# Kernel tuning notes

Hardware: AMD Instinct MI355X
Metric: run time of the kernel (lower is better)

Reference implementation:

```python
import jax, jax.numpy as jnp
import numpy as np

D, H = 64, 16
B, S = 4, 4096
PI = 3.1415  # constant used verbatim in the original code


def setup_inputs() -> dict:
    key = jax.random.key(0)
    ks = jax.random.split(key, 11)
    inp = {
        'query': jax.random.normal(ks[0], (B, S, D), dtype=jnp.float32),
        'key': jax.random.normal(ks[1], (B, S, D), dtype=jnp.float32),
        'value': jax.random.normal(ks[2], (B, S, D), dtype=jnp.float32),
        'attn_mask': jnp.zeros((1,), dtype=bool),
        # Linear weights stored as (in, out); y = x @ W + b
        'wq_w': jax.random.normal(ks[3], (D, D * H), dtype=jnp.float32) * 0.05,
        'wq_b': jnp.zeros((D * H,), dtype=jnp.float32),
        'wk_w': jax.random.normal(ks[4], (D, D * H), dtype=jnp.float32) * 0.05,
        'wk_b': jnp.zeros((D * H,), dtype=jnp.float32),
        'wv_w': jax.random.normal(ks[5], (D, D * H), dtype=jnp.float32) * 0.05,
        'wv_b': jnp.zeros((D * H,), dtype=jnp.float32),
        'dense_w': jax.random.normal(ks[6], (D * H, D), dtype=jnp.float32) * 0.05,
        'dense_b': jnp.zeros((D,), dtype=jnp.float32),
    }
    return inp


def reference(query, key, value, attn_mask, wq_w, wq_b, wk_w, wk_b, wv_w, wv_b, dense_w, dense_b):
    b, s, _ = query.shape
    # projections -> (B, S, H, D); einsum axis n = heads
    q = (query @ wq_w + wq_b).reshape(b, s, H, D)
    k = (key @ wk_w + wk_b).reshape(b, s, H, D)
    v = (value @ wv_w + wv_b).reshape(b, s, H, D)

    q = jax.nn.elu(q) + 1.0
    k = jax.nn.elu(k) + 1.0

    pos = PI * jnp.arange(s, dtype=query.dtype) / s  # (S,)
    qc_w = jnp.cos(pos)
    qs_w = jnp.sin(pos)
    kc_w = jnp.sin(pos)  # NB: original uses sin for k_cos too (faithful)
    ks_w = jnp.sin(pos)

    q_cos = q * qc_w[None, :, None, None]
    q_sin = q * qs_w[None, :, None, None]
    k_cos = k * kc_w[None, :, None, None]
    k_sin = k * ks_w[None, :, None, None]

    def lin_attn(qf, kf):
        kv = jnp.einsum('bsnx,bsnz->bnxz', kf, v)      # (B,H,D,D)
        return jnp.einsum('bsnx,bnxz->bsnz', qf, kv)   # (B,S,H,D)

    qkv = lin_attn(q, k)
    qkv_cos = lin_attn(q_cos, k_cos)
    qkv_sin = lin_attn(q_sin, k_sin)

    denom = 1.0 / (
        jnp.einsum('bsnd,bnd->bsn', q, k.sum(axis=1))
        + jnp.einsum('bsnd,bnd->bsn', q_cos, k_cos.sum(axis=1))
        + jnp.einsum('bsnd,bnd->bsn', q_sin, k_sin.sum(axis=1))
        + 1e-05
    )

    O = (qkv + qkv_cos + qkv_sin) * denom[..., None]   # (B,S,H,D)
    concat = O.reshape(b, s, H * D)
    return concat @ dense_w + dense_b
```

## Files before the change

kernel.cpp:

```cpp
#include <hip/hip_runtime.h>
#include <math.h>

#define BB 4
#define SS 4096
#define DD 64
#define HH 16
#define PI_C 3.1415f


typedef __attribute__((ext_vector_type(8))) short short8;
typedef __attribute__((ext_vector_type(4))) float f32x4;

#define MFMA(a, b, c) __builtin_amdgcn_mfma_f32_16x16x32_bf16(a, b, c, 0, 0, 0)

__device__ __forceinline__ short f2bf(float f) {
    union { float f; unsigned u; } v; v.f = f;
    unsigned r = v.u + 0x7FFFu + ((v.u >> 16) & 1u);
    return (short)(r >> 16);
}
__device__ __forceinline__ float bf2f(short s) {
    union { unsigned u; float f; } v;
    v.u = ((unsigned)(unsigned short)s) << 16;
    return v.f;
}
__device__ __forceinline__ short8 cvt8(float4 a, float4 b) {
    short8 r;
    r[0] = f2bf(a.x); r[1] = f2bf(a.y); r[2] = f2bf(a.z); r[3] = f2bf(a.w);
    r[4] = f2bf(b.x); r[5] = f2bf(b.y); r[6] = f2bf(b.z); r[7] = f2bf(b.w);
    return r;
}
__device__ __forceinline__ float elu1(float x) { return x > 0.f ? x + 1.f : __expf(x); }
__device__ __forceinline__ void st4(short* p, short a, short b, short c, short d) {
    union { uint2 u; short s[4]; } x;
    x.s[0] = a; x.s[1] = b; x.s[2] = c; x.s[3] = d;
    *reinterpret_cast<uint2*>(p) = x.u;
}

__global__ __launch_bounds__(256) void k_prep(
    const float* __restrict__ wq, const float* __restrict__ wk,
    const float* __restrict__ wv, const float* __restrict__ wd,
    short* __restrict__ dst)
{
    const int h = blockIdx.x, y = blockIdx.y, t = threadIdx.x;
    const float* src = (y == 0) ? wq : (y == 1) ? wk : (y == 2) ? wv : wd;
    const int rs = (y < 3) ? 1024 : 64;
    const size_t srcbase = (y < 3) ? (size_t)(h * 64) : (size_t)(h * 4096);
    short* dm = dst + (size_t)y * 65536 + (size_t)h * 4096;
#pragma unroll
    for (int j = 0; j < 4; ++j) {
        int idx = j * 1024 + t * 4;
        int r = idx >> 6, c = idx & 63;
        float4 v = *reinterpret_cast<const float4*>(src + (size_t)r * rs + srcbase + c);
        dm[(c + 0) * 64 + r] = f2bf(v.x);
        dm[(c + 1) * 64 + r] = f2bf(v.y);
        dm[(c + 2) * 64 + r] = f2bf(v.z);
        dm[(c + 3) * 64 + r] = f2bf(v.w);
    }
}

__global__ __launch_bounds__(256, 2) void k_phase1(
    const float* __restrict__ key, const float* __restrict__ value,
    const float* __restrict__ wk_b, const float* __restrict__ wv_b,
    const short* __restrict__ wkTb, const short* __restrict__ wvTb,
    float* __restrict__ pkv, float* __restrict__ pkvs,
    float* __restrict__ pks)
{
    const int chunk = blockIdx.x, h = blockIdx.y, b = blockIdx.z;
    const int t = threadIdx.x, w = t >> 6, l = t & 63;
    const int lane15 = l & 15, q8 = (l >> 4) * 8, q4 = (l >> 4) * 4;

    __shared__ short kT[64 * 72], vT[64 * 72], vsT[64 * 72];
    __shared__ float ssin[512];
    __shared__ float sbk[64], sbv[64];
    __shared__ float sred[512];

    short8 bkf[2][4], bvf[2][4];
    {
        const short* wkh = wkTb + (size_t)h * 4096;
        const short* wvh = wvTb + (size_t)h * 4096;
#pragma unroll
        for (int kss = 0; kss < 2; ++kss)
#pragma unroll
            for (int nt = 0; nt < 4; ++nt) {
                bkf[kss][nt] = *reinterpret_cast<const short8*>(wkh + (nt * 16 + lane15) * 64 + kss * 32 + q8);
                bvf[kss][nt] = *reinterpret_cast<const short8*>(wvh + (nt * 16 + lane15) * 64 + kss * 32 + q8);
            }
    }
    ssin[t]       = __sinf(PI_C * (float)(chunk * 512 + t)       * (1.f / 4096.f));
    ssin[t + 256] = __sinf(PI_C * (float)(chunk * 512 + t + 256) * (1.f / 4096.f));
    if (t < 64) sbk[t] = wk_b[h * 64 + t];
    else if (t < 128) sbv[t - 64] = wv_b[h * 64 + (t - 64)];

    float4 kf0, kf1, kf2, kf3, vf0, vf1, vf2, vf3;
    {
        const size_t g = ((size_t)b * SS + chunk * 512 + w * 16 + lane15) * 64 + q8;
        kf0 = *reinterpret_cast<const float4*>(key + g);
        kf1 = *reinterpret_cast<const float4*>(key + g + 4);
        kf2 = *reinterpret_cast<const float4*>(key + g + 32);
        kf3 = *reinterpret_cast<const float4*>(key + g + 36);
        vf0 = *reinterpret_cast<const float4*>(value + g);
        vf1 = *reinterpret_cast<const float4*>(value + g + 4);
        vf2 = *reinterpret_cast<const float4*>(value + g + 32);
        vf3 = *reinterpret_cast<const float4*>(value + g + 36);
    }

    f32x4 ckv[4], ckvs[4];
#pragma unroll
    for (int i = 0; i < 4; ++i) {
        ckv[i]  = (f32x4){0.f, 0.f, 0.f, 0.f};
        ckvs[i] = (f32x4){0.f, 0.f, 0.f, 0.f};
    }
    float aks = 0.f, akss = 0.f;
    __syncthreads();

    for (int it = 0; it < 8; ++it) {
        const int sbase = it * 64;
        f32x4 ckp[4], cvp[4];
#pragma unroll
        for (int i = 0; i < 4; ++i) {
            ckp[i] = (f32x4){0.f, 0.f, 0.f, 0.f};
            cvp[i] = (f32x4){0.f, 0.f, 0.f, 0.f};
        }
        {
            short8 ak0 = cvt8(kf0, kf1), ak1 = cvt8(kf2, kf3);
            short8 av0 = cvt8(vf0, vf1), av1 = cvt8(vf2, vf3);
#pragma unroll
            for (int nt = 0; nt < 4; ++nt) {
                ckp[nt] = MFMA(ak0, bkf[0][nt], ckp[nt]);
                cvp[nt] = MFMA(av0, bvf[0][nt], cvp[nt]);
                ckp[nt] = MFMA(ak1, bkf[1][nt], ckp[nt]);
                cvp[nt] = MFMA(av1, bvf[1][nt], cvp[nt]);
            }
        }
        const int srel = w * 16 + q4;
#pragma unroll
        for (int nt = 0; nt < 4; ++nt) {
            const int x = nt * 16 + lane15;
            const float bk = sbk[x], bv = sbv[x];
            short ek[4], ev[4], es[4];
#pragma unroll
            for (int r = 0; r < 4; ++r) {
                float kk = elu1(ckp[nt][r] + bk);
                float vv = cvp[nt][r] + bv;
                ek[r] = f2bf(kk);
                ev[r] = f2bf(vv);
                es[r] = f2bf(vv * ssin[sbase + srel + r]);
            }
            st4(&kT [x * 72 + srel], ek[0], ek[1], ek[2], ek[3]);
            st4(&vT [x * 72 + srel], ev[0], ev[1], ev[2], ev[3]);
            st4(&vsT[x * 72 + srel], es[0], es[1], es[2], es[3]);
        }
        __syncthreads();
        if (it < 7) {
            const size_t g = ((size_t)b * SS + chunk * 512 + (it + 1) * 64 + w * 16 + lane15) * 64 + q8;
            kf0 = *reinterpret_cast<const float4*>(key + g);
            kf1 = *reinterpret_cast<const float4*>(key + g + 4);
            kf2 = *reinterpret_cast<const float4*>(key + g + 32);
            kf3 = *reinterpret_cast<const float4*>(key + g + 36);
            vf0 = *reinterpret_cast<const float4*>(value + g);
            vf1 = *reinterpret_cast<const float4*>(value + g + 4);
            vf2 = *reinterpret_cast<const float4*>(value + g + 32);
            vf3 = *reinterpret_cast<const float4*>(value + g + 36);
        }
#pragma unroll
        for (int kstep = 0; kstep < 2; ++kstep) {
            const int so = kstep * 32;
            short8 aV  = *reinterpret_cast<const short8*>(&vT [(w * 16 + lane15) * 72 + so + q8]);
            short8 aVS = *reinterpret_cast<const short8*>(&vsT[(w * 16 + lane15) * 72 + so + q8]);
#pragma unroll
            for (int nt = 0; nt < 4; ++nt) {
                short8 bK = *reinterpret_cast<const short8*>(&kT[(nt * 16 + lane15) * 72 + so + q8]);
                ckv[nt]  = MFMA(aV,  bK, ckv[nt]);
                ckvs[nt] = MFMA(aVS, bK, ckvs[nt]);
            }
        }
        {
            short8 k0 = *reinterpret_cast<const short8*>(&kT[l * 72 + w * 16]);
            short8 k1 = *reinterpret_cast<const short8*>(&kT[l * 72 + w * 16 + 8]);
#pragma unroll
            for (int e = 0; e < 8; ++e) {
                float fa = bf2f(k0[e]), fb = bf2f(k1[e]);
                aks  += fa + fb;
                akss += fa * ssin[sbase + w * 16 + e] + fb * ssin[sbase + w * 16 + 8 + e];
            }
        }
        __syncthreads();
    }

    const int bh = b * HH + h;
    const size_t pbase = ((size_t)(chunk * 64) + bh) * 4096;
#pragma unroll
    for (int nt = 0; nt < 4; ++nt) {
        const int x = nt * 16 + lane15;
#pragma unroll
        for (int r = 0; r < 4; ++r) {
            const int z = w * 16 + q4 + r;
            pkv [pbase + z * 64 + x] = ckv[nt][r];
            pkvs[pbase + z * 64 + x] = ckvs[nt][r];
        }
    }
    sred[t] = aks; sred[256 + t] = akss;
    __syncthreads();
    if (t < 64) {
        pks[((size_t)(chunk * 64) + bh) * 128 + t] =
            sred[t] + sred[64 + t] + sred[128 + t] + sred[192 + t];
    } else if (t < 128) {
        int tt = t - 64;
        pks[((size_t)(chunk * 64) + bh) * 128 + t] =
            sred[256 + tt] + sred[320 + tt] + sred[384 + tt] + sred[448 + tt];
    }
}

__global__ __launch_bounds__(256) void k_reduce(
    const float* __restrict__ pkv, const float* __restrict__ pkvs,
    const float* __restrict__ pks,
    short* __restrict__ kvb, short* __restrict__ kvsb,
    float* __restrict__ ksums)
{
    const int blk = blockIdx.x, t = threadIdx.x;
    if (blk < 512) {
        const float* src = (blk < 256) ? pkv : pkvs;
        short* dst = (blk < 256) ? kvb : kvsb;
        const int o4 = (blk & 255) * 256 + t;
        float4 s = make_float4(0.f, 0.f, 0.f, 0.f);
#pragma unroll
        for (int c = 0; c < 8; ++c) {
            float4 v = reinterpret_cast<const float4*>(src + (size_t)c * 262144)[o4];
            s.x += v.x; s.y += v.y; s.z += v.z; s.w += v.w;
        }
        st4(dst + (size_t)o4 * 4, f2bf(s.x), f2bf(s.y), f2bf(s.z), f2bf(s.w));
    } else {
        const int g = (blk - 512) * 256 + t;
        float4 s = make_float4(0.f, 0.f, 0.f, 0.f);
#pragma unroll
        for (int c = 0; c < 8; ++c) {
            float4 v = reinterpret_cast<const float4*>(pks + (size_t)c * 8192)[g];
            s.x += v.x; s.y += v.y; s.z += v.z; s.w += v.w;
        }
        reinterpret_cast<float4*>(ksums)[g] = s;
    }
}

__global__ __launch_bounds__(256, 4) void k_phase2(
    const float* __restrict__ query, const float* __restrict__ wq_b,
    const short* __restrict__ wqTb,
    const short* __restrict__ kvb, const short* __restrict__ kvsb,
    const float* __restrict__ ksums,
    const short* __restrict__ wdTb, const float* __restrict__ dense_b,
    float* __restrict__ out)
{
    const int st = blockIdx.x, b = blockIdx.y;
    const int s0 = st * 16;
    const int t = threadIdx.x, w = t >> 6, l = t & 63;
    const int lane15 = l & 15, q8 = (l >> 4) * 8, q4 = (l >> 4) * 4;
    const int x = w * 16 + lane15;

    __shared__ short sqin[16 * 72], sqp[16 * 72], sO[16 * 72];
    __shared__ float sbq[1024];
    __shared__ float sks2[128];
    __shared__ float scc[16], sdb[64];

    if (t < 128) {
        int row = t >> 3, c8 = (t & 7) * 8;
        const float* qp = query + ((size_t)b * SS + s0 + row) * 64 + c8;
        float4 f0 = *reinterpret_cast<const float4*>(qp);
        float4 f1 = *reinterpret_cast<const float4*>(qp + 4);
        *reinterpret_cast<short8*>(&sqin[row * 72 + c8]) = cvt8(f0, f1);
    }
    for (int i = t; i < 1024; i += 256) sbq[i] = wq_b[i];
    if (t < 16) {
        float p = PI_C * (float)(s0 + t) * (1.f / 4096.f);
        scc[t] = __cosf(p) + __sinf(p);
    }
    if (t >= 192) sdb[t - 192] = dense_b[t - 192];
    f32x4 cd = (f32x4){0.f, 0.f, 0.f, 0.f};
    __syncthreads();

    for (int h = 0; h < HH; ++h) {
        const size_t bh = (size_t)(b * HH + h);
        if (t < 128) sks2[t] = ksums[bh * 128 + t];

        f32x4 cq = (f32x4){0.f, 0.f, 0.f, 0.f};
        const short* wqh = wqTb + bh % HH * 0 + (size_t)h * 4096;
#pragma unroll
        for (int kss = 0; kss < 2; ++kss) {
            short8 a = *reinterpret_cast<const short8*>(&sqin[lane15 * 72 + kss * 32 + q8]);
            short8 bb = *reinterpret_cast<const short8*>(wqh + x * 64 + kss * 32 + q8);
            cq = MFMA(a, bb, cq);
        }
        short8 nb1[2], nb2[2];
#pragma unroll
        for (int kss = 0; kss < 2; ++kss) {
            nb1[kss] = *reinterpret_cast<const short8*>(kvb  + bh * 4096 + x * 64 + kss * 32 + q8);
            nb2[kss] = *reinterpret_cast<const short8*>(kvsb + bh * 4096 + x * 64 + kss * 32 + q8);
        }
        {
            const float bq = sbq[h * 64 + x];
#pragma unroll
            for (int r = 0; r < 4; ++r)
                sqp[(q4 + r) * 72 + x] = f2bf(elu1(cq[r] + bq));
        }
        __syncthreads();

        float invd;
        {
            const int sl = l >> 2;
            const int x0 = (l & 3) * 16;
            const float ccs = scc[sl];
            short8 qa = *reinterpret_cast<const short8*>(&sqp[sl * 72 + x0]);
            short8 qb = *reinterpret_cast<const short8*>(&sqp[sl * 72 + x0 + 8]);
            float dsum = 0.f;
#pragma unroll
            for (int e = 0; e < 8; ++e) {
                dsum += bf2f(qa[e]) * (sks2[x0 + e]     + ccs * sks2[64 + x0 + e]);
                dsum += bf2f(qb[e]) * (sks2[x0 + 8 + e] + ccs * sks2[64 + x0 + 8 + e]);
            }
            dsum += __shfl_xor(dsum, 1);
            dsum += __shfl_xor(dsum, 2);
            invd = 1.f / (dsum + 1e-5f);
        }
        float invq[4], ccq[4];
#pragma unroll
        for (int r = 0; r < 4; ++r) {
            invq[r] = __shfl(invd, (q4 + r) * 4);
            ccq[r]  = scc[q4 + r];
        }

        f32x4 ckv = (f32x4){0.f, 0.f, 0.f, 0.f};
        f32x4 ckvs = (f32x4){0.f, 0.f, 0.f, 0.f};
#pragma unroll
        for (int kss = 0; kss < 2; ++kss) {
            short8 a = *reinterpret_cast<const short8*>(&sqp[lane15 * 72 + kss * 32 + q8]);
            ckv  = MFMA(a, nb1[kss], ckv);
            ckvs = MFMA(a, nb2[kss], ckvs);
        }
        short8 dbf[2];
#pragma unroll
        for (int kss = 0; kss < 2; ++kss)
            dbf[kss] = *reinterpret_cast<const short8*>(wdTb + (size_t)h * 4096 + x * 64 + kss * 32 + q8);
#pragma unroll
        for (int r = 0; r < 4; ++r) {
            float o = (ckv[r] + ccq[r] * ckvs[r]) * invq[r];
            sO[(q4 + r) * 72 + x] = f2bf(o);
        }
        __syncthreads();

#pragma unroll
        for (int kss = 0; kss < 2; ++kss) {
            short8 a = *reinterpret_cast<const short8*>(&sO[lane15 * 72 + kss * 32 + q8]);
            cd = MFMA(a, dbf[kss], cd);
        }
    }

    {
        const float bias = sdb[x];
#pragma unroll
        for (int r = 0; r < 4; ++r)
            out[((size_t)b * SS + s0 + q4 + r) * 64 + x] = cd[r] + bias;
    }
}

extern "C" void kernel_launch(void* const* d_in, const int* in_sizes, int n_in,
                              void* d_out, int out_size, void* d_ws, size_t ws_size,
                              hipStream_t stream) {
    const float* query   = (const float*)d_in[0];
    const float* key     = (const float*)d_in[1];
    const float* value   = (const float*)d_in[2];
    const float* wq_w    = (const float*)d_in[4];
    const float* wq_b    = (const float*)d_in[5];
    const float* wk_w    = (const float*)d_in[6];
    const float* wk_b    = (const float*)d_in[7];
    const float* wv_w    = (const float*)d_in[8];
    const float* wv_b    = (const float*)d_in[9];
    const float* dense_w = (const float*)d_in[10];
    const float* dense_b = (const float*)d_in[11];
    float* out = (float*)d_out;

    char* ws = (char*)d_ws;
    float* pkv   = (float*)(ws);
    float* pkvs  = (float*)(ws + 8388608);
    float* pks   = (float*)(ws + 16777216);
    short* kvb   = (short*)(ws + 17039360);
    short* kvsb  = (short*)(ws + 17563648);
    float* ksums = (float*)(ws + 18087936);
    short* wT    = (short*)(ws + 18120704);
    short* wqTb  = wT;
    short* wkTb  = wT + 65536;
    short* wvTb  = wT + 131072;
    short* wdTb  = wT + 196608;

    hipLaunchKernelGGL(k_prep, dim3(16, 4), dim3(256), 0, stream,
                       wq_w, wk_w, wv_w, dense_w, wT);
    hipLaunchKernelGGL(k_phase1, dim3(8, HH, BB), dim3(256), 0, stream,
                       key, value, wk_b, wv_b, wkTb, wvTb, pkv, pkvs, pks);
    hipLaunchKernelGGL(k_reduce, dim3(520), dim3(256), 0, stream,
                       pkv, pkvs, pks, kvb, kvsb, ksums);
    hipLaunchKernelGGL(k_phase2, dim3(256, BB), dim3(256), 0, stream,
                       query, wq_b, wqTb, kvb, kvsb, ksums, wdTb, dense_b, out);
}
```

Baseline: 173.7 us.

## Split phase1 into K/V warp groups with double-buffered LDS; per-warp heads in phase2

Phase1 now runs 512 threads per block. Four warps project and transform K while four warps handle V, and the LDS tiles are double-buffered so the next tile's projection overlaps the current kv accumulation, which removes one barrier per iteration. Phase2 no longer loops over all 16 heads with block-wide barriers. Each warp processes 4 heads independently in a private LDS buffer, computes the denominator via shuffles from preloaded ksums, and the warps' partial dense outputs are reduced through shared memory at the end. This raises LDS usage and register pressure per block, and phase2's launch bounds are loosened to 3 blocks per CU.

```diff
diff --git a/kernel.cpp b/kernel.cpp
--- a/kernel.cpp
+++ b/kernel.cpp
@@ -58,7 +58,7 @@
     }
 }
 
-__global__ __launch_bounds__(256, 2) void k_phase1(
+__global__ __launch_bounds__(512, 4) void k_phase1(
     const float* __restrict__ key, const float* __restrict__ value,
     const float* __restrict__ wk_b, const float* __restrict__ wv_b,
     const short* __restrict__ wkTb, const short* __restrict__ wvTb,
@@ -68,120 +68,145 @@
     const int chunk = blockIdx.x, h = blockIdx.y, b = blockIdx.z;
     const int t = threadIdx.x, w = t >> 6, l = t & 63;
     const int lane15 = l & 15, q8 = (l >> 4) * 8, q4 = (l >> 4) * 4;
-
-    __shared__ short kT[64 * 72], vT[64 * 72], vsT[64 * 72];
+    const int pw = w & 3;
+    const bool isV = (w >= 4);
+
+    __shared__ short kT[2][64 * 72];
+    __shared__ short vT[2][64 * 72];
+    __shared__ short vsT[2][64 * 72];
     __shared__ float ssin[512];
-    __shared__ float sbk[64], sbv[64];
-    __shared__ float sred[512];
-
-    short8 bkf[2][4], bvf[2][4];
+    __shared__ float sb[128];
+    __shared__ float sred[1024];
+
+    const short* wsrc = (isV ? wvTb : wkTb) + (size_t)h * 4096;
+    short8 bw[2][4];
+#pragma unroll
+    for (int kss = 0; kss < 2; ++kss)
+#pragma unroll
+        for (int nt = 0; nt < 4; ++nt)
+            bw[kss][nt] = *reinterpret_cast<const short8*>(
+                wsrc + (nt * 16 + lane15) * 64 + kss * 32 + q8);
+
+    ssin[t] = __sinf(PI_C * (float)(chunk * 512 + t) * (1.f / 4096.f));
+    if (t < 64) sb[t] = wk_b[h * 64 + t];
+    else if (t < 128) sb[t] = wv_b[h * 64 + (t - 64)];
+    __syncthreads();
+
+    float biasv[4];
+#pragma unroll
+    for (int nt = 0; nt < 4; ++nt)
+        biasv[nt] = sb[(isV ? 64 : 0) + nt * 16 + lane15];
+
+    const float* gsrc = isV ? value : key;
+    const int scol = pw * 16 + q4;
+
+    float4 f0, f1, f2, f3;
     {
-        const short* wkh = wkTb + (size_t)h * 4096;
-        const short* wvh = wvTb + (size_t)h * 4096;
-#pragma unroll
-        for (int kss = 0; kss < 2; ++kss)
+        const size_t g = ((size_t)b * SS + chunk * 512 + pw * 16 + lane15) * 64 + q8;
+        f0 = *reinterpret_cast<const float4*>(gsrc + g);
+        f1 = *reinterpret_cast<const float4*>(gsrc + g + 4);
+        f2 = *reinterpret_cast<const float4*>(gsrc + g + 32);
+        f3 = *reinterpret_cast<const float4*>(gsrc + g + 36);
+    }
+    {
+        short8 a0 = cvt8(f0, f1), a1 = cvt8(f2, f3);
+        f32x4 cp[4];
+#pragma unroll
+        for (int nt = 0; nt < 4; ++nt) cp[nt] = (f32x4){0.f, 0.f, 0.f, 0.f};
+#pragma unroll
+        for (int nt = 0; nt < 4; ++nt) {
+            cp[nt] = MFMA(a0, bw[0][nt], cp[nt]);
+            cp[nt] = MFMA(a1, bw[1][nt], cp[nt]);
+        }
+#pragma unroll
+        for (int nt = 0; nt < 4; ++nt) {
+            const int x = nt * 16 + lane15;
+            if (!isV) {
+                short e[4];
+#pragma unroll
+                for (int r = 0; r < 4; ++r) e[r] = f2bf(elu1(cp[nt][r] + biasv[nt]));
+                st4(&kT[0][x * 72 + scol], e[0], e[1], e[2], e[3]);
+            } else {
+                short ev[4], es[4];
+#pragma unroll
+                for (int r = 0; r < 4; ++r) {
+                    float vv = cp[nt][r] + biasv[nt];
+                    ev[r] = f2bf(vv);
+                    es[r] = f2bf(vv * ssin[scol + r]);
+                }
+                st4(&vT[0][x * 72 + scol], ev[0], ev[1], ev[2], ev[3]);
+                st4(&vsT[0][x * 72 + scol], es[0], es[1], es[2], es[3]);
+            }
+        }
+    }
+    __syncthreads();
+
+    f32x4 cacc[4];
+#pragma unroll
+    for (int nt = 0; nt < 4; ++nt) cacc[nt] = (f32x4){0.f, 0.f, 0.f, 0.f};
+    float aks = 0.f, akss = 0.f;
+
+    for (int it = 0; it < 8; ++it) {
+        const int p = it & 1;
+        if (it < 7) {
+            const size_t g = ((size_t)b * SS + chunk * 512 + (it + 1) * 64 + pw * 16 + lane15) * 64 + q8;
+            f0 = *reinterpret_cast<const float4*>(gsrc + g);
+            f1 = *reinterpret_cast<const float4*>(gsrc + g + 4);
+            f2 = *reinterpret_cast<const float4*>(gsrc + g + 32);
+            f3 = *reinterpret_cast<const float4*>(gsrc + g + 36);
+        }
+        {
+            const short* At = isV ? vsT[p] : vT[p];
+            short8 a0 = *reinterpret_cast<const short8*>(&At[(pw * 16 + lane15) * 72 + q8]);
+            short8 a1 = *reinterpret_cast<const short8*>(&At[(pw * 16 + lane15) * 72 + 32 + q8]);
 #pragma unroll
             for (int nt = 0; nt < 4; ++nt) {
-                bkf[kss][nt] = *reinterpret_cast<const short8*>(wkh + (nt * 16 + lane15) * 64 + kss * 32 + q8);
-                bvf[kss][nt] = *reinterpret_cast<const short8*>(wvh + (nt * 16 + lane15) * 64 + kss * 32 + q8);
-            }
-    }
-    ssin[t]       = __sinf(PI_C * (float)(chunk * 512 + t)       * (1.f / 4096.f));
-    ssin[t + 256] = __sinf(PI_C * (float)(chunk * 512 + t + 256) * (1.f / 4096.f));
-    if (t < 64) sbk[t] = wk_b[h * 64 + t];
-    else if (t < 128) sbv[t - 64] = wv_b[h * 64 + (t - 64)];
-
-    float4 kf0, kf1, kf2, kf3, vf0, vf1, vf2, vf3;
-    {
-        const size_t g = ((size_t)b * SS + chunk * 512 + w * 16 + lane15) * 64 + q8;
-        kf0 = *reinterpret_cast<const float4*>(key + g);
-        kf1 = *reinterpret_cast<const float4*>(key + g + 4);
-        kf2 = *reinterpret_cast<const float4*>(key + g + 32);
-        kf3 = *reinterpret_cast<const float4*>(key + g + 36);
-        vf0 = *reinterpret_cast<const float4*>(value + g);
-        vf1 = *reinterpret_cast<const float4*>(value + g + 4);
-        vf2 = *reinterpret_cast<const float4*>(value + g + 32);
-        vf3 = *reinterpret_cast<const float4*>(value + g + 36);
-    }
-
-    f32x4 ckv[4], ckvs[4];
-#pragma unroll
-    for (int i = 0; i < 4; ++i) {
-        ckv[i]  = (f32x4){0.f, 0.f, 0.f, 0.f};
-        ckvs[i] = (f32x4){0.f, 0.f, 0.f, 0.f};
-    }
-    float aks = 0.f, akss = 0.f;
-    __syncthreads();
-
-    for (int it = 0; it < 8; ++it) {
-        const int sbase = it * 64;
-        f32x4 ckp[4], cvp[4];
-#pragma unroll
-        for (int i = 0; i < 4; ++i) {
-            ckp[i] = (f32x4){0.f, 0.f, 0.f, 0.f};
-            cvp[i] = (f32x4){0.f, 0.f, 0.f, 0.f};
+                short8 b0 = *reinterpret_cast<const short8*>(&kT[p][(nt * 16 + lane15) * 72 + q8]);
+                short8 b1 = *reinterpret_cast<const short8*>(&kT[p][(nt * 16 + lane15) * 72 + 32 + q8]);
+                cacc[nt] = MFMA(a0, b0, cacc[nt]);
+                cacc[nt] = MFMA(a1, b1, cacc[nt]);
+            }
         }
         {
-            short8 ak0 = cvt8(kf0, kf1), ak1 = cvt8(kf2, kf3);
-            short8 av0 = cvt8(vf0, vf1), av1 = cvt8(vf2, vf3);
+            short8 kk = *reinterpret_cast<const short8*>(&kT[p][l * 72 + w * 8]);
+#pragma unroll
+            for (int e = 0; e < 8; ++e) {
+                float f = bf2f(kk[e]);
+                aks += f;
+                akss = fmaf(f, ssin[it * 64 + w * 8 + e], akss);
+            }
+        }
+        if (it < 7) {
+            short8 a0 = cvt8(f0, f1), a1 = cvt8(f2, f3);
+            f32x4 cp[4];
+#pragma unroll
+            for (int nt = 0; nt < 4; ++nt) cp[nt] = (f32x4){0.f, 0.f, 0.f, 0.f};
 #pragma unroll
             for (int nt = 0; nt < 4; ++nt) {
-                ckp[nt] = MFMA(ak0, bkf[0][nt], ckp[nt]);
-                cvp[nt] = MFMA(av0, bvf[0][nt], cvp[nt]);
-                ckp[nt] = MFMA(ak1, bkf[1][nt], ckp[nt]);
-                cvp[nt] = MFMA(av1, bvf[1][nt], cvp[nt]);
-            }
-        }
-        const int srel = w * 16 + q4;
-#pragma unroll
-        for (int nt = 0; nt < 4; ++nt) {
-            const int x = nt * 16 + lane15;
-            const float bk = sbk[x], bv = sbv[x];
-            short ek[4], ev[4], es[4];
-#pragma unroll
-            for (int r = 0; r < 4; ++r) {
-                float kk = elu1(ckp[nt][r] + bk);
-                float vv = cvp[nt][r] + bv;
-                ek[r] = f2bf(kk);
-                ev[r] = f2bf(vv);
-                es[r] = f2bf(vv * ssin[sbase + srel + r]);
-            }
-            st4(&kT [x * 72 + srel], ek[0], ek[1], ek[2], ek[3]);
-            st4(&vT [x * 72 + srel], ev[0], ev[1], ev[2], ev[3]);
-            st4(&vsT[x * 72 + srel], es[0], es[1], es[2], es[3]);
-        }
-        __syncthreads();
-        if (it < 7) {
-            const size_t g = ((size_t)b * SS + chunk * 512 + (it + 1) * 64 + w * 16 + lane15) * 64 + q8;
-            kf0 = *reinterpret_cast<const float4*>(key + g);
-            kf1 = *reinterpret_cast<const float4*>(key + g + 4);
-            kf2 = *reinterpret_cast<const float4*>(key + g + 32);
-            kf3 = *reinterpret_cast<const float4*>(key + g + 36);
-            vf0 = *reinterpret_cast<const float4*>(value + g);
-            vf1 = *reinterpret_cast<const float4*>(value + g + 4);
-            vf2 = *reinterpret_cast<const float4*>(value + g + 32);
-            vf3 = *reinterpret_cast<const float4*>(value + g + 36);
-        }
-#pragma unroll
-        for (int kstep = 0; kstep < 2; ++kstep) {
-            const int so = kstep * 32;
-            short8 aV  = *reinterpret_cast<const short8*>(&vT [(w * 16 + lane15) * 72 + so + q8]);
-            short8 aVS = *reinterpret_cast<const short8*>(&vsT[(w * 16 + lane15) * 72 + so + q8]);
+                cp[nt] = MFMA(a0, bw[0][nt], cp[nt]);
+                cp[nt] = MFMA(a1, bw[1][nt], cp[nt]);
+            }
+            const int pn = p ^ 1;
+            const int sabs = (it + 1) * 64 + scol;
 #pragma unroll
             for (int nt = 0; nt < 4; ++nt) {
-                short8 bK = *reinterpret_cast<const short8*>(&kT[(nt * 16 + lane15) * 72 + so + q8]);
-                ckv[nt]  = MFMA(aV,  bK, ckv[nt]);
-                ckvs[nt] = MFMA(aVS, bK, ckvs[nt]);
-            }
-        }
-        {
-            short8 k0 = *reinterpret_cast<const short8*>(&kT[l * 72 + w * 16]);
-            short8 k1 = *reinterpret_cast<const short8*>(&kT[l * 72 + w * 16 + 8]);
-#pragma unroll
-            for (int e = 0; e < 8; ++e) {
-                float fa = bf2f(k0[e]), fb = bf2f(k1[e]);
-                aks  += fa + fb;
-                akss += fa * ssin[sbase + w * 16 + e] + fb * ssin[sbase + w * 16 + 8 + e];
+                const int x = nt * 16 + lane15;
+                if (!isV) {
+                    short e[4];
+#pragma unroll
+                    for (int r = 0; r < 4; ++r) e[r] = f2bf(elu1(cp[nt][r] + biasv[nt]));
+                    st4(&kT[pn][x * 72 + scol], e[0], e[1], e[2], e[3]);
+                } else {
+                    short ev[4], es[4];
+#pragma unroll
+                    for (int r = 0; r < 4; ++r) {
+                        float vv = cp[nt][r] + biasv[nt];
+                        ev[r] = f2bf(vv);
+                        es[r] = f2bf(vv * ssin[sabs + r]);
+                    }
+                    st4(&vT[pn][x * 72 + scol], ev[0], ev[1], ev[2], ev[3]);
+                    st4(&vsT[pn][x * 72 + scol], es[0], es[1], es[2], es[3]);
+                }
             }
         }
         __syncthreads();
@@ -189,25 +214,29 @@
 
     const int bh = b * HH + h;
     const size_t pbase = ((size_t)(chunk * 64) + bh) * 4096;
+    float* dst = isV ? pkvs : pkv;
 #pragma unroll
     for (int nt = 0; nt < 4; ++nt) {
         const int x = nt * 16 + lane15;
 #pragma unroll
         for (int r = 0; r < 4; ++r) {
-            const int z = w * 16 + q4 + r;
-            pkv [pbase + z * 64 + x] = ckv[nt][r];
-            pkvs[pbase + z * 64 + x] = ckvs[nt][r];
-        }
-    }
-    sred[t] = aks; sred[256 + t] = akss;
+            const int z = pw * 16 + q4 + r;
+            dst[pbase + z * 64 + x] = cacc[nt][r];
+        }
+    }
+    sred[t] = aks; sred[512 + t] = akss;
     __syncthreads();
     if (t < 64) {
-        pks[((size_t)(chunk * 64) + bh) * 128 + t] =
-            sred[t] + sred[64 + t] + sred[128 + t] + sred[192 + t];
+        float s = 0.f;
+#pragma unroll
+        for (int j = 0; j < 8; ++j) s += sred[j * 64 + t];
+        pks[((size_t)(chunk * 64) + bh) * 128 + t] = s;
     } else if (t < 128) {
-        int tt = t - 64;
-        pks[((size_t)(chunk * 64) + bh) * 128 + t] =
-            sred[256 + tt] + sred[320 + tt] + sred[384 + tt] + sred[448 + tt];
+        const int tt = t - 64;
+        float s = 0.f;
+#pragma unroll
+        for (int j = 0; j < 8; ++j) s += sred[512 + j * 64 + tt];
+        pks[((size_t)(chunk * 64) + bh) * 128 + t] = s;
     }
 }
 
@@ -241,7 +270,7 @@
     }
 }
 
-__global__ __launch_bounds__(256, 4) void k_phase2(
+__global__ __launch_bounds__(256, 3) void k_phase2(
     const float* __restrict__ query, const float* __restrict__ wq_b,
     const short* __restrict__ wqTb,
     const short* __restrict__ kvb, const short* __restrict__ kvsb,
@@ -253,110 +282,144 @@
     const int s0 = st * 16;
     const int t = threadIdx.x, w = t >> 6, l = t & 63;
     const int lane15 = l & 15, q8 = (l >> 4) * 8, q4 = (l >> 4) * 4;
-    const int x = w * 16 + lane15;
-
-    __shared__ short sqin[16 * 72], sqp[16 * 72], sO[16 * 72];
+
+    __shared__ short sqin[16 * 72];
+    __shared__ short wbuf[4][16 * 72];
     __shared__ float sbq[1024];
-    __shared__ float sks2[128];
-    __shared__ float scc[16], sdb[64];
+    __shared__ float sksall[16 * 128];
+    __shared__ float scc[16];
+    __shared__ float sdb[64];
+    __shared__ float sred[4][16 * 68];
 
     if (t < 128) {
         int row = t >> 3, c8 = (t & 7) * 8;
         const float* qp = query + ((size_t)b * SS + s0 + row) * 64 + c8;
-        float4 f0 = *reinterpret_cast<const float4*>(qp);
-        float4 f1 = *reinterpret_cast<const float4*>(qp + 4);
-        *reinterpret_cast<short8*>(&sqin[row * 72 + c8]) = cvt8(f0, f1);
+        float4 g0 = *reinterpret_cast<const float4*>(qp);
+        float4 g1 = *reinterpret_cast<const float4*>(qp + 4);
+        *reinterpret_cast<short8*>(&sqin[row * 72 + c8]) = cvt8(g0, g1);
     }
     for (int i = t; i < 1024; i += 256) sbq[i] = wq_b[i];
+    {
+        const float4* src = reinterpret_cast<const float4*>(ksums + (size_t)b * 2048);
+        reinterpret_cast<float4*>(sksall)[t] = src[t];
+        reinterpret_cast<float4*>(sksall)[t + 256] = src[t + 256];
+    }
     if (t < 16) {
         float p = PI_C * (float)(s0 + t) * (1.f / 4096.f);
         scc[t] = __cosf(p) + __sinf(p);
     }
     if (t >= 192) sdb[t - 192] = dense_b[t - 192];
-    f32x4 cd = (f32x4){0.f, 0.f, 0.f, 0.f};
     __syncthreads();
 
-    for (int h = 0; h < HH; ++h) {
+    float ccr[4];
+#pragma unroll
+    for (int r = 0; r < 4; ++r) ccr[r] = scc[q4 + r];
+
+    short* myb = &wbuf[w][0];
+    f32x4 cd[4];
+#pragma unroll
+    for (int nt = 0; nt < 4; ++nt) cd[nt] = (f32x4){0.f, 0.f, 0.f, 0.f};
+
+    for (int hh = 0; hh < 4; ++hh) {
+        const int h = hh * 4 + w;
         const size_t bh = (size_t)(b * HH + h);
-        if (t < 128) sks2[t] = ksums[bh * 128 + t];
-
-        f32x4 cq = (f32x4){0.f, 0.f, 0.f, 0.f};
-        const short* wqh = wqTb + bh % HH * 0 + (size_t)h * 4096;
-#pragma unroll
-        for (int kss = 0; kss < 2; ++kss) {
-            short8 a = *reinterpret_cast<const short8*>(&sqin[lane15 * 72 + kss * 32 + q8]);
-            short8 bb = *reinterpret_cast<const short8*>(wqh + x * 64 + kss * 32 + q8);
-            cq = MFMA(a, bb, cq);
-        }
-        short8 nb1[2], nb2[2];
-#pragma unroll
-        for (int kss = 0; kss < 2; ++kss) {
-            nb1[kss] = *reinterpret_cast<const short8*>(kvb  + bh * 4096 + x * 64 + kss * 32 + q8);
-            nb2[kss] = *reinterpret_cast<const short8*>(kvsb + bh * 4096 + x * 64 + kss * 32 + q8);
-        }
-        {
+        const short* wqh = wqTb + (size_t)h * 4096;
+
+        short8 aq0 = *reinterpret_cast<const short8*>(&sqin[lane15 * 72 + q8]);
+        short8 aq1 = *reinterpret_cast<const short8*>(&sqin[lane15 * 72 + 32 + q8]);
+        f32x4 cq[4];
+#pragma unroll
+        for (int nt = 0; nt < 4; ++nt) cq[nt] = (f32x4){0.f, 0.f, 0.f, 0.f};
+#pragma unroll
+        for (int nt = 0; nt < 4; ++nt) {
+            short8 b0 = *reinterpret_cast<const short8*>(wqh + (nt * 16 + lane15) * 64 + q8);
+            short8 b1 = *reinterpret_cast<const short8*>(wqh + (nt * 16 + lane15) * 64 + 32 + q8);
+            cq[nt] = MFMA(aq0, b0, cq[nt]);
+            cq[nt] = MFMA(aq1, b1, cq[nt]);
+        }
+        float dp[4] = {0.f, 0.f, 0.f, 0.f};
+#pragma unroll
+        for (int nt = 0; nt < 4; ++nt) {
+            const int x = nt * 16 + lane15;
             const float bq = sbq[h * 64 + x];
-#pragma unroll
-            for (int r = 0; r < 4; ++r)
-                sqp[(q4 + r) * 72 + x] = f2bf(elu1(cq[r] + bq));
-        }
-        __syncthreads();
-
-        float invd;
-        {
-            const int sl = l >> 2;
-            const int x0 = (l & 3) * 16;
-            const float ccs = scc[sl];
-            short8 qa = *reinterpret_cast<const short8*>(&sqp[sl * 72 + x0]);
-            short8 qb = *reinterpret_cast<const short8*>(&sqp[sl * 72 + x0 + 8]);
-            float dsum = 0.f;
-#pragma unroll
-            for (int e = 0; e < 8; ++e) {
-                dsum += bf2f(qa[e]) * (sks2[x0 + e]     + ccs * sks2[64 + x0 + e]);
-                dsum += bf2f(qb[e]) * (sks2[x0 + 8 + e] + ccs * sks2[64 + x0 + 8 + e]);
-            }
-            dsum += __shfl_xor(dsum, 1);
-            dsum += __shfl_xor(dsum, 2);
-            invd = 1.f / (dsum + 1e-5f);
-        }
-        float invq[4], ccq[4];
-#pragma unroll
-        for (int r = 0; r < 4; ++r) {
-            invq[r] = __shfl(invd, (q4 + r) * 4);
-            ccq[r]  = scc[q4 + r];
-        }
-
-        f32x4 ckv = (f32x4){0.f, 0.f, 0.f, 0.f};
-        f32x4 ckvs = (f32x4){0.f, 0.f, 0.f, 0.f};
-#pragma unroll
-        for (int kss = 0; kss < 2; ++kss) {
-            short8 a = *reinterpret_cast<const short8*>(&sqp[lane15 * 72 + kss * 32 + q8]);
-            ckv  = MFMA(a, nb1[kss], ckv);
-            ckvs = MFMA(a, nb2[kss], ckvs);
-        }
-        short8 dbf[2];
-#pragma unroll
-        for (int kss = 0; kss < 2; ++kss)
-            dbf[kss] = *reinterpret_cast<const short8*>(wdTb + (size_t)h * 4096 + x * 64 + kss * 32 + q8);
-#pragma unroll
-        for (int r = 0; r < 4; ++r) {
-            float o = (ckv[r] + ccq[r] * ckvs[r]) * invq[r];
-            sO[(q4 + r) * 72 + x] = f2bf(o);
-        }
-        __syncthreads();
-
-#pragma unroll
-        for (int kss = 0; kss < 2; ++kss) {
-            short8 a = *reinterpret_cast<const short8*>(&sO[lane15 * 72 + kss * 32 + q8]);
-            cd = MFMA(a, dbf[kss], cd);
-        }
-    }
-
+            const float ksx = sksall[h * 128 + x];
+            const float kssx = sksall[h * 128 + 64 + x];
+#pragma unroll
+            for (int r = 0; r < 4; ++r) {
+                float qv = elu1(cq[nt][r] + bq);
+                dp[r] = fmaf(qv, fmaf(ccr[r], kssx, ksx), dp[r]);
+                myb[(q4 + r) * 72 + x] = f2bf(qv);
+            }
+        }
+#pragma unroll
+        for (int m = 1; m <= 8; m <<= 1) {
+#pragma unroll
+            for (int r = 0; r < 4; ++r) dp[r] += __shfl_xor(dp[r], m);
+        }
+        float invd[4];
+#pragma unroll
+        for (int r = 0; r < 4; ++r) invd[r] = 1.f / (dp[r] + 1e-5f);
+
+        const short* kvh  = kvb  + bh * 4096;
+        const short* kvsh = kvsb + bh * 4096;
+        short8 a20 = *reinterpret_cast<const short8*>(&myb[lane15 * 72 + q8]);
+        short8 a21 = *reinterpret_cast<const short8*>(&myb[lane15 * 72 + 32 + q8]);
+        f32x4 ckv[4], ckvs[4];
+#pragma unroll
+        for (int nt = 0; nt < 4; ++nt) {
+            ckv[nt] = (f32x4){0.f, 0.f, 0.f, 0.f};
+            ckvs[nt] = (f32x4){0.f, 0.f, 0.f, 0.f};
+        }
+#pragma unroll
+        for (int nt = 0; nt < 4; ++nt) {
+            short8 b0 = *reinterpret_cast<const short8*>(kvh + (nt * 16 + lane15) * 64 + q8);
+            short8 b1 = *reinterpret_cast<const short8*>(kvh + (nt * 16 + lane15) * 64 + 32 + q8);
+            short8 c0 = *reinterpret_cast<const short8*>(kvsh + (nt * 16 + lane15) * 64 + q8);
+            short8 c1 = *reinterpret_cast<const short8*>(kvsh + (nt * 16 + lane15) * 64 + 32 + q8);
+            ckv[nt]  = MFMA(a20, b0, ckv[nt]);
+            ckv[nt]  = MFMA(a21, b1, ckv[nt]);
+            ckvs[nt] = MFMA(a20, c0, ckvs[nt]);
+            ckvs[nt] = MFMA(a21, c1, ckvs[nt]);
+        }
+#pragma unroll
+        for (int nt = 0; nt < 4; ++nt) {
+            const int z = nt * 16 + lane15;
+#pragma unroll
+            for (int r = 0; r < 4; ++r) {
+                float o = fmaf(ccr[r], ckvs[nt][r], ckv[nt][r]) * invd[r];
+                myb[(q4 + r) * 72 + z] = f2bf(o);
+            }
+        }
+        const short* wdh = wdTb + (size_t)h * 4096;
+        short8 a30 = *reinterpret_cast<const short8*>(&myb[lane15 * 72 + q8]);
+        short8 a31 = *reinterpret_cast<const short8*>(&myb[lane15 * 72 + 32 + q8]);
+#pragma unroll
+        for (int nt = 0; nt < 4; ++nt) {
+            short8 b0 = *reinterpret_cast<const short8*>(wdh + (nt * 16 + lane15) * 64 + q8);
+            short8 b1 = *reinterpret_cast<const short8*>(wdh + (nt * 16 + lane15) * 64 + 32 + q8);
+            cd[nt] = MFMA(a30, b0, cd[nt]);
+            cd[nt] = MFMA(a31, b1, cd[nt]);
+        }
+    }
+
+#pragma unroll
+    for (int nt = 0; nt < 4; ++nt) {
+#pragma unroll
+        for (int r = 0; r < 4; ++r)
+            sred[w][(q4 + r) * 68 + nt * 16 + lane15] = cd[nt][r];
+    }
+    __syncthreads();
     {
-        const float bias = sdb[x];
-#pragma unroll
-        for (int r = 0; r < 4; ++r)
-            out[((size_t)b * SS + s0 + q4 + r) * 64 + x] = cd[r] + bias;
+        const int row = t >> 4, c0 = (t & 15) * 4;
+        float4 s = make_float4(0.f, 0.f, 0.f, 0.f);
+#pragma unroll
+        for (int j = 0; j < 4; ++j) {
+            float4 v = *reinterpret_cast<const float4*>(&sred[j][row * 68 + c0]);
+            s.x += v.x; s.y += v.y; s.z += v.z; s.w += v.w;
+        }
+        float4 db = *reinterpret_cast<const float4*>(&sdb[c0]);
+        s.x += db.x; s.y += db.y; s.z += db.z; s.w += db.w;
+        *reinterpret_cast<float4*>(out + ((size_t)b * SS + s0 + row) * 64 + c0) = s;
     }
 }
 
@@ -391,7 +454,7 @@
 
     hipLaunchKernelGGL(k_prep, dim3(16, 4), dim3(256), 0, stream,
                        wq_w, wk_w, wv_w, dense_w, wT);
-    hipLaunchKernelGGL(k_phase1, dim3(8, HH, BB), dim3(256), 0, stream,
+    hipLaunchKernelGGL(k_phase1, dim3(8, HH, BB), dim3(512), 0, stream,
                        key, value, wk_b, wv_b, wkTb, wvTb, pkv, pkvs, pks);
     hipLaunchKernelGGL(k_reduce, dim3(520), dim3(256), 0, stream,
                        pkv, pkvs, pks, kvb, kvsb, ksums);
```

Result: slower. 206.3 us (+18.8%).

## Split phase-2 across head groups with per-wave heads and partial-sum reduction kernel

Applied to the files above, without the earlier changes.

Replaces the serial 16-head loop in phase 2 with a grid over 4 head groups. Each wave handles one head end to end without block-level syncs, keeping the intermediate tiles in a per-wave LDS buffer. The four wave partials are reduced in LDS and written to a workspace buffer, and a new small kernel sums the group partials and adds the dense bias. This raises parallelism (four times as many blocks) and removes the per-head __syncthreads, at the cost of extra global traffic for the partial sums and one more launch.

```diff
diff --git a/kernel.cpp b/kernel.cpp
--- a/kernel.cpp
+++ b/kernel.cpp
@@ -241,123 +241,167 @@
     }
 }
 
-__global__ __launch_bounds__(256, 4) void k_phase2(
+__global__ __launch_bounds__(256, 2) void k_attn(
     const float* __restrict__ query, const float* __restrict__ wq_b,
     const short* __restrict__ wqTb,
     const short* __restrict__ kvb, const short* __restrict__ kvsb,
     const float* __restrict__ ksums,
-    const short* __restrict__ wdTb, const float* __restrict__ dense_b,
-    float* __restrict__ out)
+    const short* __restrict__ wdTb,
+    float* __restrict__ pden)
 {
-    const int st = blockIdx.x, b = blockIdx.y;
+    const int st = blockIdx.x, g = blockIdx.y, b = blockIdx.z;
     const int s0 = st * 16;
     const int t = threadIdx.x, w = t >> 6, l = t & 63;
     const int lane15 = l & 15, q8 = (l >> 4) * 8, q4 = (l >> 4) * 4;
-    const int x = w * 16 + lane15;
-
-    __shared__ short sqin[16 * 72], sqp[16 * 72], sO[16 * 72];
-    __shared__ float sbq[1024];
-    __shared__ float sks2[128];
-    __shared__ float scc[16], sdb[64];
-
-    if (t < 128) {
-        int row = t >> 3, c8 = (t & 7) * 8;
-        const float* qp = query + ((size_t)b * SS + s0 + row) * 64 + c8;
-        float4 f0 = *reinterpret_cast<const float4*>(qp);
-        float4 f1 = *reinterpret_cast<const float4*>(qp + 4);
-        *reinterpret_cast<short8*>(&sqin[row * 72 + c8]) = cvt8(f0, f1);
-    }
-    for (int i = t; i < 1024; i += 256) sbq[i] = wq_b[i];
-    if (t < 16) {
-        float p = PI_C * (float)(s0 + t) * (1.f / 4096.f);
-        scc[t] = __cosf(p) + __sinf(p);
-    }
-    if (t >= 192) sdb[t - 192] = dense_b[t - 192];
-    f32x4 cd = (f32x4){0.f, 0.f, 0.f, 0.f};
+    const int h = g * 4 + w;
+    const size_t bh = (size_t)(b * HH + h);
+
+    __shared__ short wbuf[4][16 * 72];
+    __shared__ float sred[4][16 * 68];
+
+    short* myb = &wbuf[w][0];
+
+    float ccr[4];
+#pragma unroll
+    for (int r = 0; r < 4; ++r) {
+        float p = PI_C * (float)(s0 + q4 + r) * (1.f / 4096.f);
+        ccr[r] = __cosf(p) + __sinf(p);
+    }
+
+    const float* qrow = query + ((size_t)b * SS + s0 + lane15) * 64;
+    short8 aq0, aq1;
+    {
+        float4 f0 = *reinterpret_cast<const float4*>(qrow + q8);
+        float4 f1 = *reinterpret_cast<const float4*>(qrow + q8 + 4);
+        float4 f2 = *reinterpret_cast<const float4*>(qrow + 32 + q8);
+        float4 f3 = *reinterpret_cast<const float4*>(qrow + 32 + q8 + 4);
+        aq0 = cvt8(f0, f1);
+        aq1 = cvt8(f2, f3);
+    }
+
+    f32x4 cq[4];
+#pragma unroll
+    for (int nt = 0; nt < 4; ++nt) cq[nt] = (f32x4){0.f, 0.f, 0.f, 0.f};
+    {
+        const short* wqh = wqTb + (size_t)h * 4096;
+#pragma unroll
+        for (int nt = 0; nt < 4; ++nt) {
+            short8 b0 = *reinterpret_cast<const short8*>(wqh + (nt * 16 + lane15) * 64 + q8);
+            short8 b1 = *reinterpret_cast<const short8*>(wqh + (nt * 16 + lane15) * 64 + 32 + q8);
+            cq[nt] = MFMA(aq0, b0, cq[nt]);
+            cq[nt] = MFMA(aq1, b1, cq[nt]);
+        }
+    }
+
+    float dp[4] = {0.f, 0.f, 0.f, 0.f};
+#pragma unroll
+    for (int nt = 0; nt < 4; ++nt) {
+        const int x = nt * 16 + lane15;
+        const float bq = wq_b[h * 64 + x];
+        const float ksx = ksums[bh * 128 + x];
+        const float kssx = ksums[bh * 128 + 64 + x];
+#pragma unroll
+        for (int r = 0; r < 4; ++r) {
+            float qv = elu1(cq[nt][r] + bq);
+            dp[r] = fmaf(qv, fmaf(ccr[r], kssx, ksx), dp[r]);
+            myb[(q4 + r) * 72 + x] = f2bf(qv);
+        }
+    }
+#pragma unroll
+    for (int m = 1; m <= 8; m <<= 1) {
+#pragma unroll
+        for (int r = 0; r < 4; ++r) dp[r] += __shfl_xor(dp[r], m);
+    }
+    float invd[4];
+#pragma unroll
+    for (int r = 0; r < 4; ++r) invd[r] = 1.f / (dp[r] + 1e-5f);
+
+    short8 a20 = *reinterpret_cast<const short8*>(&myb[lane15 * 72 + q8]);
+    short8 a21 = *reinterpret_cast<const short8*>(&myb[lane15 * 72 + 32 + q8]);
+
+    f32x4 ckv[4], ckvs[4];
+#pragma unroll
+    for (int nt = 0; nt < 4; ++nt) {
+        ckv[nt]  = (f32x4){0.f, 0.f, 0.f, 0.f};
+        ckvs[nt] = (f32x4){0.f, 0.f, 0.f, 0.f};
+    }
+    {
+        const short* kvh  = kvb  + bh * 4096;
+        const short* kvsh = kvsb + bh * 4096;
+#pragma unroll
+        for (int nt = 0; nt < 4; ++nt) {
+            short8 b0 = *reinterpret_cast<const short8*>(kvh + (nt * 16 + lane15) * 64 + q8);
+            short8 b1 = *reinterpret_cast<const short8*>(kvh + (nt * 16 + lane15) * 64 + 32 + q8);
+            short8 c0 = *reinterpret_cast<const short8*>(kvsh + (nt * 16 + lane15) * 64 + q8);
+            short8 c1 = *reinterpret_cast<const short8*>(kvsh + (nt * 16 + lane15) * 64 + 32 + q8);
+            ckv[nt]  = MFMA(a20, b0, ckv[nt]);
+            ckv[nt]  = MFMA(a21, b1, ckv[nt]);
+            ckvs[nt] = MFMA(a20, c0, ckvs[nt]);
+            ckvs[nt] = MFMA(a21, c1, ckvs[nt]);
+        }
+    }
+
+#pragma unroll
+    for (int nt = 0; nt < 4; ++nt) {
+        const int z = nt * 16 + lane15;
+#pragma unroll
+        for (int r = 0; r < 4; ++r) {
+            float o = fmaf(ccr[r], ckvs[nt][r], ckv[nt][r]) * invd[r];
+            myb[(q4 + r) * 72 + z] = f2bf(o);
+        }
+    }
+    short8 a30 = *reinterpret_cast<const short8*>(&myb[lane15 * 72 + q8]);
+    short8 a31 = *reinterpret_cast<const short8*>(&myb[lane15 * 72 + 32 + q8]);
+
+    f32x4 cd[4];
+#pragma unroll
+    for (int nt = 0; nt < 4; ++nt) cd[nt] = (f32x4){0.f, 0.f, 0.f, 0.f};
+    {
+        const short* wdh = wdTb + (size_t)h * 4096;
+#pragma unroll
+        for (int nt = 0; nt < 4; ++nt) {
+            short8 b0 = *reinterpret_cast<const short8*>(wdh + (nt * 16 + lane15) * 64 + q8);
+            short8 b1 = *reinterpret_cast<const short8*>(wdh + (nt * 16 + lane15) * 64 + 32 + q8);
+            cd[nt] = MFMA(a30, b0, cd[nt]);
+            cd[nt] = MFMA(a31, b1, cd[nt]);
+        }
+    }
+
+#pragma unroll
+    for (int nt = 0; nt < 4; ++nt) {
+#pragma unroll
+        for (int r = 0; r < 4; ++r)
+            sred[w][(q4 + r) * 68 + nt * 16 + lane15] = cd[nt][r];
+    }
     __syncthreads();
-
-    for (int h = 0; h < HH; ++h) {
-        const size_t bh = (size_t)(b * HH + h);
-        if (t < 128) sks2[t] = ksums[bh * 128 + t];
-
-        f32x4 cq = (f32x4){0.f, 0.f, 0.f, 0.f};
-        const short* wqh = wqTb + bh % HH * 0 + (size_t)h * 4096;
-#pragma unroll
-        for (int kss = 0; kss < 2; ++kss) {
-            short8 a = *reinterpret_cast<const short8*>(&sqin[lane15 * 72 + kss * 32 + q8]);
-            short8 bb = *reinterpret_cast<const short8*>(wqh + x * 64 + kss * 32 + q8);
-            cq = MFMA(a, bb, cq);
-        }
-        short8 nb1[2], nb2[2];
-#pragma unroll
-        for (int kss = 0; kss < 2; ++kss) {
-            nb1[kss] = *reinterpret_cast<const short8*>(kvb  + bh * 4096 + x * 64 + kss * 32 + q8);
-            nb2[kss] = *reinterpret_cast<const short8*>(kvsb + bh * 4096 + x * 64 + kss * 32 + q8);
-        }
-        {
-            const float bq = sbq[h * 64 + x];
-#pragma unroll
-            for (int r = 0; r < 4; ++r)
-                sqp[(q4 + r) * 72 + x] = f2bf(elu1(cq[r] + bq));
-        }
-        __syncthreads();
-
-        float invd;
-        {
-            const int sl = l >> 2;
-            const int x0 = (l & 3) * 16;
-            const float ccs = scc[sl];
-            short8 qa = *reinterpret_cast<const short8*>(&sqp[sl * 72 + x0]);
-            short8 qb = *reinterpret_cast<const short8*>(&sqp[sl * 72 + x0 + 8]);
-            float dsum = 0.f;
-#pragma unroll
-            for (int e = 0; e < 8; ++e) {
-                dsum += bf2f(qa[e]) * (sks2[x0 + e]     + ccs * sks2[64 + x0 + e]);
-                dsum += bf2f(qb[e]) * (sks2[x0 + 8 + e] + ccs * sks2[64 + x0 + 8 + e]);
-            }
-            dsum += __shfl_xor(dsum, 1);
-            dsum += __shfl_xor(dsum, 2);
-            invd = 1.f / (dsum + 1e-5f);
-        }
-        float invq[4], ccq[4];
-#pragma unroll
-        for (int r = 0; r < 4; ++r) {
-            invq[r] = __shfl(invd, (q4 + r) * 4);
-            ccq[r]  = scc[q4 + r];
-        }
-
-        f32x4 ckv = (f32x4){0.f, 0.f, 0.f, 0.f};
-        f32x4 ckvs = (f32x4){0.f, 0.f, 0.f, 0.f};
-#pragma unroll
-        for (int kss = 0; kss < 2; ++kss) {
-            short8 a = *reinterpret_cast<const short8*>(&sqp[lane15 * 72 + kss * 32 + q8]);
-            ckv  = MFMA(a, nb1[kss], ckv);
-            ckvs = MFMA(a, nb2[kss], ckvs);
-        }
-        short8 dbf[2];
-#pragma unroll
-        for (int kss = 0; kss < 2; ++kss)
-            dbf[kss] = *reinterpret_cast<const short8*>(wdTb + (size_t)h * 4096 + x * 64 + kss * 32 + q8);
-#pragma unroll
-        for (int r = 0; r < 4; ++r) {
-            float o = (ckv[r] + ccq[r] * ckvs[r]) * invq[r];
-            sO[(q4 + r) * 72 + x] = f2bf(o);
-        }
-        __syncthreads();
-
-#pragma unroll
-        for (int kss = 0; kss < 2; ++kss) {
-            short8 a = *reinterpret_cast<const short8*>(&sO[lane15 * 72 + kss * 32 + q8]);
-            cd = MFMA(a, dbf[kss], cd);
-        }
-    }
-
-    {
-        const float bias = sdb[x];
-#pragma unroll
-        for (int r = 0; r < 4; ++r)
-            out[((size_t)b * SS + s0 + q4 + r) * 64 + x] = cd[r] + bias;
-    }
+    {
+        const int row = t >> 4, c0 = (t & 15) * 4;
+        float4 s = make_float4(0.f, 0.f, 0.f, 0.f);
+#pragma unroll
+        for (int j = 0; j < 4; ++j) {
+            float4 v = *reinterpret_cast<const float4*>(&sred[j][row * 68 + c0]);
+            s.x += v.x; s.y += v.y; s.z += v.z; s.w += v.w;
+        }
+        *reinterpret_cast<float4*>(
+            pden + (((size_t)(g * BB + b) * SS) + s0 + row) * 64 + c0) = s;
+    }
+}
+
+__global__ __launch_bounds__(256) void k_dfinal(
+    const float* __restrict__ pden, const float* __restrict__ dense_b,
+    float* __restrict__ out)
+{
+    const int i4 = blockIdx.x * 256 + threadIdx.x;
+    const int c4 = i4 & 15;
+    const int bb = i4 >> 16;
+    const int rem = i4 & 65535;
+    float4 s = *reinterpret_cast<const float4*>(dense_b + c4 * 4);
+#pragma unroll
+    for (int g = 0; g < 4; ++g) {
+        float4 v = reinterpret_cast<const float4*>(pden)[(size_t)(g * BB + bb) * 65536 + rem];
+        s.x += v.x; s.y += v.y; s.z += v.z; s.w += v.w;
+    }
+    reinterpret_cast<float4*>(out)[i4] = s;
 }
 
 extern "C" void kernel_launch(void* const* d_in, const int* in_sizes, int n_in,
@@ -379,6 +423,7 @@
     char* ws = (char*)d_ws;
     float* pkv   = (float*)(ws);
     float* pkvs  = (float*)(ws + 8388608);
+    float* pden  = (float*)(ws);
     float* pks   = (float*)(ws + 16777216);
     short* kvb   = (short*)(ws + 17039360);
     short* kvsb  = (short*)(ws + 17563648);
@@ -395,6 +440,8 @@
                        key, value, wk_b, wv_b, wkTb, wvTb, pkv, pkvs, pks);
     hipLaunchKernelGGL(k_reduce, dim3(520), dim3(256), 0, stream,
                        pkv, pkvs, pks, kvb, kvsb, ksums);
-    hipLaunchKernelGGL(k_phase2, dim3(256, BB), dim3(256), 0, stream,
-                       query, wq_b, wqTb, kvb, kvsb, ksums, wdTb, dense_b, out);
-}
+    hipLaunchKernelGGL(k_attn, dim3(SS / 16, 4, BB), dim3(256), 0, stream,
+                       query, wq_b, wqTb, kvb, kvsb, ksums, wdTb, pden);
+    hipLaunchKernelGGL(k_dfinal, dim3(1024), dim3(256), 0, stream,
+                       pden, dense_b, out);
+}
```

Measured after the change: 185.9 us. +7.1%, slower.
